# Kernel tuning notes

Measured on AMD Instinct MI355X. Metric: run time of the kernel, lower is better.

The kernel has to match this reference:

```python
import jax, jax.numpy as jnp
import numpy as np

# static config
B, H, W, C = 32, 56, 56, 128
WH, WW = 7, 7
SH, SW = 3, 3
NH = 4            # num heads
HD = C // NH      # head dim = 32
N = WH * WW       # 49 tokens per window
NWIN = (H // WH) * (W // WW)  # 64 windows
MLP_H = int(C * 4.0)
EPS = 1e-6
SCALE = HD ** -0.5


def _rel_pos_index():
    ch, cw = np.arange(WH), np.arange(WW)
    co = np.stack(np.meshgrid(ch, cw, indexing='ij')).reshape(2, -1)
    rc = (co[:, :, None] - co[:, None, :]).transpose(1, 2, 0)
    rc[:, :, 0] += WH - 1
    rc[:, :, 1] += WW - 1
    rc[:, :, 0] *= 2 * WW - 1
    return rc.sum(-1)  # [N, N] int


def _attn_mask():
    img = np.zeros((1, H, W, 1), np.float32)
    cnt = 0
    for hs in (slice(0, -WH), slice(-WH, -SH), slice(-SH, None)):
        for ws in (slice(0, -WW), slice(-WW, -SW), slice(-SW, None)):
            img[:, hs, ws, :] = cnt
            cnt += 1
    mw = img.reshape(1, H // WH, WH, W // WW, WW, 1)
    mw = mw.transpose(0, 1, 3, 2, 4, 5).reshape(-1, N)  # [nW, N]
    am = mw[:, None, :] - mw[:, :, None]
    return np.where(am != 0, -100.0, 0.0).astype(np.float32)  # [nW, N, N]

REL_IDX = jnp.asarray(_rel_pos_index())
ATTN_MASK = jnp.asarray(_attn_mask())


def _ln(x, g, b):
    mu = jnp.mean(x, -1, keepdims=True)
    var = jnp.mean(jnp.square(x - mu), -1, keepdims=True)
    return (x - mu) * jax.lax.rsqrt(var + EPS) * g + b


def _part(x):  # [B,H,W,C] -> [B*nW, N, C]
    x = x.reshape(B, H // WH, WH, W // WW, WW, C)
    return x.transpose(0, 1, 3, 2, 4, 5).reshape(-1, N, C)


def _rev(w):  # [B*nW, N, C] -> [B,H,W,C]
    x = w.reshape(B, H // WH, W // WW, WH, WW, C)
    return x.transpose(0, 1, 3, 2, 4, 5).reshape(B, H, W, C)


def setup_inputs() -> dict:
    key = jax.random.key(0)
    ks = jax.random.split(key, 16)
    s = lambda k, sh, sc=0.02: jax.random.normal(k, sh, jnp.float32) * sc
    return {
        'x': jax.random.normal(ks[0], (B, H * W, C), jnp.float32),
        'qkv_w': s(ks[1], (C, 3 * C)),
        'qkv_b': jnp.zeros((3 * C,), jnp.float32),
        'proj_w': s(ks[2], (C, C)),
        'proj_b': jnp.zeros((C,), jnp.float32),
        'proj_ln_g': jnp.ones((C,), jnp.float32),
        'proj_ln_b': jnp.zeros((C,), jnp.float32),
        'rpb_table': s(ks[3], ((2 * WH - 1) * (2 * WW - 1), NH)),
        'norm1_g': jnp.ones((C,), jnp.float32),
        'norm1_b': jnp.zeros((C,), jnp.float32),
        'norm2_g': jnp.ones((C,), jnp.float32),
        'norm2_b': jnp.zeros((C,), jnp.float32),
        'mlp_w1': s(ks[4], (C, MLP_H)),
        'mlp_b1': jnp.zeros((MLP_H,), jnp.float32),
        'mlp_w2': s(ks[5], (MLP_H, C)),
        'mlp_b2': jnp.zeros((C,), jnp.float32),
    }


def reference(x, qkv_w, qkv_b, proj_w, proj_b, proj_ln_g, proj_ln_b, rpb_table,
              norm1_g, norm1_b, norm2_g, norm2_b, mlp_w1, mlp_b1, mlp_w2, mlp_b2):
    shortcut = x
    h = _ln(x, norm1_g, norm1_b).reshape(B, H, W, C)
    h = jnp.roll(h, shift=(-SH, -SW), axis=(1, 2))        # cyclic shift
    w = _part(h)                                          # [B*nW, N, C]

    qkv = w @ qkv_w + qkv_b                               # [B*nW, N, 3C]
    qkv = qkv.reshape(-1, N, 3, NH, HD).transpose(2, 0, 3, 1, 4)
    q, k, v = qkv[0] * SCALE, qkv[1], qkv[2]              # [B*nW, NH, N, HD]
    attn = jnp.einsum('bhnd,bhmd->bhnm', q, k)            # [B*nW, NH, N, N]

    bias = rpb_table[REL_IDX.reshape(-1)].reshape(N, N, NH).transpose(2, 0, 1)
    attn = attn + bias[None]

    # masked path (shifted windows): NOTE source applies softmax TWICE — faithful
    attn = attn.reshape(-1, NWIN, NH, N, N) + ATTN_MASK[None, :, None]
    attn = jax.nn.softmax(attn, axis=-1)
    attn = attn.reshape(-1, NH, N, N)
    attn = jax.nn.softmax(attn, axis=-1)

    o = jnp.einsum('bhnm,bhmd->bhnd', attn, v)
    o = o.transpose(0, 2, 1, 3).reshape(-1, N, C)
    # projection: Dense -> LayerNorm -> GELU (as in source WindowAttention)
    o = jax.nn.gelu(_ln(o @ proj_w + proj_b, proj_ln_g, proj_ln_b), approximate=False)

    h = _rev(o)
    h = jnp.roll(h, shift=(SH, SW), axis=(1, 2)).reshape(B, H * W, C)
    x = shortcut + h

    m = _ln(x, norm2_g, norm2_b)
    m = jax.nn.gelu(m @ mlp_w1 + mlp_b1, approximate=False) @ mlp_w2 + mlp_b2
    return x + m
```

## Files before the change

kernel.cpp:

```cpp
#include <hip/hip_runtime.h>
#include <cstdint>
#include <cstddef>

typedef __attribute__((ext_vector_type(8))) short bf16x8;
typedef __attribute__((ext_vector_type(4))) float f32x4;

namespace {
constexpr float kScale = 0.17677669529663689f;
constexpr float kEps = 1e-6f;
constexpr float kInvC = 1.0f / 128.0f;

__device__ __forceinline__ float gelu_fast(float v) {
  float t1 = fmaf(0.044715f * v, v, 1.0f);
  float x = v * t1 * -1.5957691216057308f;
  float e = __expf(x);
  return v * __builtin_amdgcn_rcpf(1.0f + e);
}
__device__ __forceinline__ ushort f2bf(float f) {
  uint32_t u = __builtin_bit_cast(uint32_t, f);
  u += 0x7FFFu + ((u >> 16) & 1u);
  return (ushort)(u >> 16);
}
__device__ __forceinline__ float bf2f(ushort u) {
  return __builtin_bit_cast(float, (uint32_t)u << 16);
}
__device__ __forceinline__ void gl16(const ushort* g, ushort* l) {
  __builtin_amdgcn_global_load_lds(
      (const __attribute__((address_space(1))) void*)g,
      (__attribute__((address_space(3))) void*)l, 16, 0, 0);
}
__device__ __forceinline__ int map_row(int t) {
  int win = t / 49, nn = t - win * 49;
  int bb = win >> 6, wi = win & 63;
  int whi = wi >> 3, wwi = wi & 7;
  int r7 = nn / 7, c7 = nn - r7 * 7;
  int hs = whi * 7 + r7 + 3; if (hs >= 56) hs -= 56;
  int wsd = wwi * 7 + c7 + 3; if (wsd >= 56) wsd -= 56;
  return bb * 3136 + hs * 56 + wsd;
}
}

__global__ __launch_bounds__(256) void k_prep(
    const float* __restrict__ qkv_w, const float* __restrict__ w1,
    const float* __restrict__ w2, const float* __restrict__ pw,
    ushort* __restrict__ qkvT, ushort* __restrict__ w1T,
    ushort* __restrict__ w2T, ushort* __restrict__ projT) {
  int i = blockIdx.x * 256 + threadIdx.x;
  if (i < 49152) {
    int n = i >> 7, k = i & 127;
    qkvT[i] = f2bf(qkv_w[k * 384 + n]);
  } else if (i < 114688) {
    int j = i - 49152;
    int n = j >> 7, k = j & 127;
    w1T[j] = f2bf(w1[k * 512 + n]);
  } else if (i < 180224) {
    int j = i - 114688;
    int n = j >> 9, k = j & 511;
    w2T[j] = f2bf(w2[k * 128 + n]);
  } else if (i < 196608) {
    int j = i - 180224;
    int n = j >> 7, k = j & 127;
    projT[j] = f2bf(pw[k * 128 + n]);
  }
}

__global__ __launch_bounds__(256) void k_prep2(
    const float* __restrict__ rpb, float* __restrict__ TB) {
  int e = blockIdx.x * 256 + threadIdx.x;
  int i = e & 63, j = (e >> 6) & 63, h = (e >> 12) & 3, type = e >> 14;
  float v = 0.f;
  if (i < 49 && j < 49) {
    int ri = i / 7, ci = i - ri * 7, rj = j / 7, cj = j - rj * 7;
    int ridx = (ri - rj + 6) * 13 + (ci - cj + 6);
    float bias = rpb[ridx * 4 + h];
    int th = type >> 1, tw = type & 1;
    int labi = (th ? ((ri < 4) ? 1 : 2) : 0) * 3 + (tw ? ((ci < 4) ? 1 : 2) : 0);
    int labj = (th ? ((rj < 4) ? 1 : 2) : 0) * 3 + (tw ? ((cj < 4) ? 1 : 2) : 0);
    v = bias + ((labi != labj) ? -100.f : 0.f);
  }
  TB[e] = v;
}

__global__ __launch_bounds__(256) void k_ln1_part(
    const float* __restrict__ x, const float* __restrict__ g,
    const float* __restrict__ b, ushort* __restrict__ wp) {
  int lane = threadIdx.x & 63, wv = threadIdx.x >> 6;
  int half = lane >> 5, l32 = lane & 31;
  int tok = blockIdx.x * 8 + wv * 2 + half;
  size_t src = (size_t)map_row(tok) * 128;
  float4 v = *(const float4*)(x + src + l32 * 4);
  float s = v.x + v.y + v.z + v.w;
  float sq = v.x * v.x + v.y * v.y + v.z * v.z + v.w * v.w;
#pragma unroll
  for (int off = 1; off < 32; off <<= 1) {
    s += __shfl_xor(s, off);
    sq += __shfl_xor(sq, off);
  }
  float mu = s * kInvC;
  float var = sq * kInvC - mu * mu;
  float rs = rsqrtf(var + kEps);
  float4 gg = *(const float4*)(g + l32 * 4);
  float4 bv = *(const float4*)(b + l32 * 4);
  float o0 = (v.x - mu) * rs * gg.x + bv.x;
  float o1 = (v.y - mu) * rs * gg.y + bv.y;
  float o2 = (v.z - mu) * rs * gg.z + bv.z;
  float o3 = (v.w - mu) * rs * gg.w + bv.w;
  uint2 p;
  p.x = (uint)f2bf(o0) | ((uint)f2bf(o1) << 16);
  p.y = (uint)f2bf(o2) | ((uint)f2bf(o3) << 16);
  ((uint2*)wp)[(size_t)tok * 32 + l32] = p;
}

template <int K, int LDC, int EPI>
__global__ __launch_bounds__(256) void k_gemm2(
    const ushort* __restrict__ A, const ushort* __restrict__ BT,
    const float* __restrict__ bias, ushort* __restrict__ C) {
  __shared__ ushort sbuf[12288];
  int tid = threadIdx.x;
  int nBase = blockIdx.x << 7;
  int mBase = blockIdx.y << 6;
  int lane = tid & 63, wid = tid >> 6;
  int li = lane & 15, g = lane >> 4;
  int wr = (wid >> 1) << 5, wc = (wid & 1) << 6;
  int swz = (li & 7) << 3;
  f32x4 acc[2][4] = {};
  for (int ks = 0; ks < K; ks += 64) {
#pragma unroll
    for (int l = 0; l < 2; ++l) {
      int c = l * 256 + tid;
      int row = c >> 3;
      int k8 = ((c & 7) ^ (row & 7)) << 3;
      gl16(A + (size_t)(mBase + row) * K + ks + k8,
           sbuf + (l * 256 + wid * 64) * 8);
    }
#pragma unroll
    for (int l = 0; l < 4; ++l) {
      int c = l * 256 + tid;
      int row = c >> 3;
      int k8 = ((c & 7) ^ (row & 7)) << 3;
      gl16(BT + (size_t)(nBase + row) * K + ks + k8,
           sbuf + 4096 + (l * 256 + wid * 64) * 8);
    }
    __syncthreads();
#pragma unroll
    for (int ksub = 0; ksub < 64; ksub += 32) {
      int kloc = ksub + g * 8;
      bf16x8 af[2], bfr[4];
#pragma unroll
      for (int m = 0; m < 2; ++m)
        af[m] = *(const bf16x8*)(sbuf + (wr + m * 16 + li) * 64 + (kloc ^ swz));
#pragma unroll
      for (int n = 0; n < 4; ++n)
        bfr[n] = *(const bf16x8*)(sbuf + 4096 + (wc + n * 16 + li) * 64 +
                                  (kloc ^ swz));
#pragma unroll
      for (int m = 0; m < 2; ++m)
#pragma unroll
        for (int n = 0; n < 4; ++n)
          acc[m][n] = __builtin_amdgcn_mfma_f32_16x16x32_bf16(
              af[m], bfr[n], acc[m][n], 0, 0, 0);
    }
    __syncthreads();
  }
  ushort (*Cs)[128] = (ushort(*)[128])sbuf;
#pragma unroll
  for (int n = 0; n < 4; ++n) {
    float bv = bias[nBase + wc + n * 16 + li];
#pragma unroll
    for (int m = 0; m < 2; ++m) {
      int rb = wr + m * 16 + (g << 2);
#pragma unroll
      for (int r = 0; r < 4; ++r) {
        float v = acc[m][n][r] + bv;
        if (EPI == 1) v = gelu_fast(v);
        Cs[rb + r][wc + n * 16 + li] = f2bf(v);
      }
    }
  }
  __syncthreads();
#pragma unroll
  for (int it = 0; it < 4; ++it) {
    int ch = tid + it * 256;
    int row = ch >> 4, c8 = (ch & 15) << 3;
    *(bf16x8*)(C + (size_t)(mBase + row) * LDC + nBase + c8) =
        *(const bf16x8*)&Cs[row][c8];
  }
}

__global__ __launch_bounds__(256) void k_mlp2(
    const ushort* __restrict__ A, const ushort* __restrict__ BT,
    const float* __restrict__ bias, const ushort* __restrict__ resw,
    float* __restrict__ out) {
  __shared__ ushort sbuf[16384];
  __shared__ int mapr[64];
  int tid = threadIdx.x;
  int mBase = blockIdx.x << 6;
  if (tid < 64) mapr[tid] = map_row(mBase + tid);
  int lane = tid & 63, wid = tid >> 6;
  int li = lane & 15, g = lane >> 4;
  int wr = (wid >> 1) << 5, wc = (wid & 1) << 6;
  int swz = (li & 7) << 3;
  f32x4 acc[2][4] = {};
  for (int ks = 0; ks < 512; ks += 64) {
#pragma unroll
    for (int l = 0; l < 2; ++l) {
      int c = l * 256 + tid;
      int row = c >> 3;
      int k8 = ((c & 7) ^ (row & 7)) << 3;
      gl16(A + (size_t)(mBase + row) * 512 + ks + k8,
           sbuf + (l * 256 + wid * 64) * 8);
    }
#pragma unroll
    for (int l = 0; l < 4; ++l) {
      int c = l * 256 + tid;
      int row = c >> 3;
      int k8 = ((c & 7) ^ (row & 7)) << 3;
      gl16(BT + (size_t)row * 512 + ks + k8,
           sbuf + 4096 + (l * 256 + wid * 64) * 8);
    }
    __syncthreads();
#pragma unroll
    for (int ksub = 0; ksub < 64; ksub += 32) {
      int kloc = ksub + g * 8;
      bf16x8 af[2], bfr[4];
#pragma unroll
      for (int m = 0; m < 2; ++m)
        af[m] = *(const bf16x8*)(sbuf + (wr + m * 16 + li) * 64 + (kloc ^ swz));
#pragma unroll
      for (int n = 0; n < 4; ++n)
        bfr[n] = *(const bf16x8*)(sbuf + 4096 + (wc + n * 16 + li) * 64 +
                                  (kloc ^ swz));
#pragma unroll
      for (int m = 0; m < 2; ++m)
#pragma unroll
        for (int n = 0; n < 4; ++n)
          acc[m][n] = __builtin_amdgcn_mfma_f32_16x16x32_bf16(
              af[m], bfr[n], acc[m][n], 0, 0, 0);
    }
    __syncthreads();
  }
  float (*outs)[128] = (float(*)[128])sbuf;
#pragma unroll
  for (int n = 0; n < 4; ++n) {
    int cg = wc + n * 16 + li;
    float bv = bias[cg];
#pragma unroll
    for (int m = 0; m < 2; ++m) {
      int rb = wr + m * 16 + (g << 2);
#pragma unroll
      for (int r = 0; r < 4; ++r) {
        float rv = bf2f(resw[(size_t)(mBase + rb + r) * 128 + cg]);
        outs[rb + r][cg] = rv + acc[m][n][r] + bv;
      }
    }
  }
  __syncthreads();
#pragma unroll
  for (int it = 0; it < 8; ++it) {
    int ch = tid + it * 256;
    int row = ch >> 5, c4 = (ch & 31) << 2;
    *(float4*)(out + (size_t)mapr[row] * 128 + c4) =
        *(const float4*)&outs[row][c4];
  }
}

__global__ __launch_bounds__(256) void k_pgemm(
    const ushort* __restrict__ A, const ushort* __restrict__ BT,
    const float* __restrict__ pb, const float* __restrict__ lg,
    const float* __restrict__ lb, const float* __restrict__ x,
    const float* __restrict__ g2, const float* __restrict__ b2n,
    ushort* __restrict__ resw, ushort* __restrict__ wp) {
  __shared__ ushort sbuf[16384];
  __shared__ float red[4][64][2];
  __shared__ int mapr[64];
  int tid = threadIdx.x;
  int mBase = blockIdx.x << 6;
  if (tid < 64) mapr[tid] = map_row(mBase + tid);
  int lane = tid & 63, wid = tid >> 6;
  int li = lane & 15, g = lane >> 4;
  int wr = (wid >> 1) << 5, wc = (wid & 1) << 6;
  int swz = (li & 7) << 3;
  f32x4 acc[2][4] = {};
  for (int ks = 0; ks < 128; ks += 64) {
#pragma unroll
    for (int l = 0; l < 2; ++l) {
      int c = l * 256 + tid;
      int row = c >> 3;
      int k8 = ((c & 7) ^ (row & 7)) << 3;
      gl16(A + (size_t)(mBase + row) * 128 + ks + k8,
           sbuf + (l * 256 + wid * 64) * 8);
    }
#pragma unroll
    for (int l = 0; l < 4; ++l) {
      int c = l * 256 + tid;
      int row = c >> 3;
      int k8 = ((c & 7) ^ (row & 7)) << 3;
      gl16(BT + (size_t)row * 128 + ks + k8,
           sbuf + 4096 + (l * 256 + wid * 64) * 8);
    }
    __syncthreads();
#pragma unroll
    for (int ksub = 0; ksub < 64; ksub += 32) {
      int kloc = ksub + g * 8;
      bf16x8 af[2], bfr[4];
#pragma unroll
      for (int m = 0; m < 2; ++m)
        af[m] = *(const bf16x8*)(sbuf + (wr + m * 16 + li) * 64 + (kloc ^ swz));
#pragma unroll
      for (int n = 0; n < 4; ++n)
        bfr[n] = *(const bf16x8*)(sbuf + 4096 + (wc + n * 16 + li) * 64 +
                                  (kloc ^ swz));
#pragma unroll
      for (int m = 0; m < 2; ++m)
#pragma unroll
        for (int n = 0; n < 4; ++n)
          acc[m][n] = __builtin_amdgcn_mfma_f32_16x16x32_bf16(
              af[m], bfr[n], acc[m][n], 0, 0, 0);
    }
    __syncthreads();
  }
  float pbv[4], lgv[4], lbv[4], g2v[4], b2v[4];
#pragma unroll
  for (int n = 0; n < 4; ++n) {
    int cg = wc + n * 16 + li;
    pbv[n] = pb[cg]; lgv[n] = lg[cg]; lbv[n] = lb[cg];
    g2v[n] = g2[cg]; b2v[n] = b2n[cg];
  }
  float ps[2][4], psq[2][4];
#pragma unroll
  for (int m = 0; m < 2; ++m)
#pragma unroll
    for (int r = 0; r < 4; ++r) {
      float s = 0.f, q = 0.f;
#pragma unroll
      for (int n = 0; n < 4; ++n) {
        float v = acc[m][n][r] + pbv[n];
        s += v; q += v * v;
      }
#pragma unroll
      for (int off = 1; off < 16; off <<= 1) {
        s += __shfl_xor(s, off);
        q += __shfl_xor(q, off);
      }
      ps[m][r] = s; psq[m][r] = q;
    }
  if (li == 0) {
#pragma unroll
    for (int m = 0; m < 2; ++m)
#pragma unroll
      for (int r = 0; r < 4; ++r) {
        int rl = wr + m * 16 + (g << 2) + r;
        red[wid][rl][0] = ps[m][r];
        red[wid][rl][1] = psq[m][r];
      }
  }
  __syncthreads();
  float mu1[2][4], rs1[2][4];
#pragma unroll
  for (int m = 0; m < 2; ++m)
#pragma unroll
    for (int r = 0; r < 4; ++r) {
      int rl = wr + m * 16 + (g << 2) + r;
      float s = ps[m][r] + red[wid ^ 1][rl][0];
      float q = psq[m][r] + red[wid ^ 1][rl][1];
      mu1[m][r] = s * kInvC;
      rs1[m][r] = rsqrtf(q * kInvC - mu1[m][r] * mu1[m][r] + kEps);
    }
  __syncthreads();
#pragma unroll
  for (int m = 0; m < 2; ++m)
#pragma unroll
    for (int r = 0; r < 4; ++r) {
      int rowl = wr + m * 16 + (g << 2) + r;
      size_t xb = (size_t)mapr[rowl] * 128 + wc + li;
#pragma unroll
      for (int n = 0; n < 4; ++n) {
        float y = (acc[m][n][r] + pbv[n] - mu1[m][r]) * rs1[m][r] * lgv[n] +
                  lbv[n];
        acc[m][n][r] = gelu_fast(y) + x[xb + n * 16];
      }
    }
#pragma unroll
  for (int m = 0; m < 2; ++m)
#pragma unroll
    for (int r = 0; r < 4; ++r) {
      float s = 0.f, q = 0.f;
#pragma unroll
      for (int n = 0; n < 4; ++n) {
        float v = acc[m][n][r];
        s += v; q += v * v;
      }
#pragma unroll
      for (int off = 1; off < 16; off <<= 1) {
        s += __shfl_xor(s, off);
        q += __shfl_xor(q, off);
      }
      ps[m][r] = s; psq[m][r] = q;
    }
  if (li == 0) {
#pragma unroll
    for (int m = 0; m < 2; ++m)
#pragma unroll
      for (int r = 0; r < 4; ++r) {
        int rl = wr + m * 16 + (g << 2) + r;
        red[wid][rl][0] = ps[m][r];
        red[wid][rl][1] = psq[m][r];
      }
  }
  __syncthreads();
  ushort (*Cr)[128] = (ushort(*)[128])sbuf;
  ushort (*Cw)[128] = (ushort(*)[128])(sbuf + 8192);
#pragma unroll
  for (int m = 0; m < 2; ++m)
#pragma unroll
    for (int r = 0; r < 4; ++r) {
      int rl = wr + m * 16 + (g << 2) + r;
      float s = ps[m][r] + red[wid ^ 1][rl][0];
      float q = psq[m][r] + red[wid ^ 1][rl][1];
      float mu = s * kInvC;
      float rs = rsqrtf(q * kInvC - mu * mu + kEps);
#pragma unroll
      for (int n = 0; n < 4; ++n) {
        int col = wc + n * 16 + li;
        float rv = acc[m][n][r];
        Cr[rl][col] = f2bf(rv);
        Cw[rl][col] = f2bf((rv - mu) * rs * g2v[n] + b2v[n]);
      }
    }
  __syncthreads();
#pragma unroll
  for (int it = 0; it < 4; ++it) {
    int ch = tid + it * 256;
    int row = ch >> 4, c8 = (ch & 15) << 3;
    *(bf16x8*)(resw + (size_t)(mBase + row) * 128 + c8) =
        *(const bf16x8*)&Cr[row][c8];
    *(bf16x8*)(wp + (size_t)(mBase + row) * 128 + c8) =
        *(const bf16x8*)&Cw[row][c8];
  }
}

__global__ __launch_bounds__(256) void k_attn(
    const ushort* __restrict__ qkv, const float* __restrict__ TB,
    ushort* __restrict__ ob) {
  __shared__ ushort Pl[4][64][72];
  __shared__ ushort Vt[4][32][72];
  int tid = threadIdx.x;
  int lane = tid & 63, h = tid >> 6;
  int li = lane & 15, g = lane >> 4;
  int win = blockIdx.x;
  int wi = win & 63;
  int type = (((wi >> 3) == 7) ? 2 : 0) | (((wi & 7) == 7) ? 1 : 0);

  const ushort* qbase = qkv + (size_t)win * 49 * 384 + h * 32 + g * 8;
  bf16x8 kf[4], qf[4];
#pragma unroll
  for (int m = 0; m < 4; ++m) {
    kf[m] = *(const bf16x8*)(qbase + (size_t)(m * 16 + li) * 384 + 128);
    qf[m] = *(const bf16x8*)(qbase + (size_t)(m * 16 + li) * 384);
  }
  f32x4 zero = {0.f, 0.f, 0.f, 0.f};
  f32x4 st[4][4];
#pragma unroll
  for (int m = 0; m < 4; ++m)
#pragma unroll
    for (int n = 0; n < 4; ++n)
      st[m][n] = __builtin_amdgcn_mfma_f32_16x16x32_bf16(kf[m], qf[n], zero, 0, 0, 0);

  if (lane < 49) {
#pragma unroll
    for (int dc = 0; dc < 4; ++dc) {
      bf16x8 vv = *(const bf16x8*)(qkv + ((size_t)win * 49 + lane) * 384 + 256 +
                                   h * 32 + dc * 8);
#pragma unroll
      for (int t = 0; t < 8; ++t) Vt[h][dc * 8 + t][lane] = (ushort)vv[t];
    }
  } else {
#pragma unroll
    for (int d = 0; d < 32; ++d) Vt[h][d][lane] = 0;
  }

  const float* tb = TB + ((size_t)(type * 4 + h) << 12);
#pragma unroll
  for (int n = 0; n < 4; ++n) {
    int icol = n * 16 + li;
    float sv[3][4];
#pragma unroll
    for (int m = 0; m < 3; ++m)
#pragma unroll
      for (int r = 0; r < 4; ++r)
        sv[m][r] = st[m][n][r] * kScale + tb[(m * 16 + g * 4 + r) * 64 + icol];
    float sv3 = (g == 0) ? (st[3][n][0] * kScale + tb[48 * 64 + icol]) : -1e30f;
    float mx = sv3;
#pragma unroll
    for (int m = 0; m < 3; ++m)
#pragma unroll
      for (int r = 0; r < 4; ++r) mx = fmaxf(mx, sv[m][r]);
    mx = fmaxf(mx, __shfl_xor(mx, 16));
    mx = fmaxf(mx, __shfl_xor(mx, 32));
    float e[3][4], e3 = __expf(sv3 - mx);
    float sum = e3;
#pragma unroll
    for (int m = 0; m < 3; ++m)
#pragma unroll
      for (int r = 0; r < 4; ++r) { e[m][r] = __expf(sv[m][r] - mx); sum += e[m][r]; }
    sum += __shfl_xor(sum, 16);
    sum += __shfl_xor(sum, 32);
    float inv = 1.f / sum;
    float p3 = e3 * inv;
    float v3 = (g == 0) ? p3 : -1e30f;
    float mx2 = v3;
#pragma unroll
    for (int m = 0; m < 3; ++m)
#pragma unroll
      for (int r = 0; r < 4; ++r) mx2 = fmaxf(mx2, e[m][r] * inv);
    mx2 = fmaxf(mx2, __shfl_xor(mx2, 16));
    mx2 = fmaxf(mx2, __shfl_xor(mx2, 32));
    float e2[3][4], e23 = __expf(v3 - mx2);
    float sum2 = e23;
#pragma unroll
    for (int m = 0; m < 3; ++m)
#pragma unroll
      for (int r = 0; r < 4; ++r) { e2[m][r] = __expf(e[m][r] * inv - mx2); sum2 += e2[m][r]; }
    sum2 += __shfl_xor(sum2, 16);
    sum2 += __shfl_xor(sum2, 32);
    float inv2 = 1.f / sum2;
#pragma unroll
    for (int m = 0; m < 3; ++m) {
      uint u0 = (uint)f2bf(e2[m][0] * inv2) | ((uint)f2bf(e2[m][1] * inv2) << 16);
      uint u1 = (uint)f2bf(e2[m][2] * inv2) | ((uint)f2bf(e2[m][3] * inv2) << 16);
      *(uint*)&Pl[h][icol][m * 16 + g * 4]     = u0;
      *(uint*)&Pl[h][icol][m * 16 + g * 4 + 2] = u1;
    }
    uint u3 = (uint)f2bf(e23 * inv2);
    *(uint*)&Pl[h][icol][48 + g * 4]     = u3;
    *(uint*)&Pl[h][icol][48 + g * 4 + 2] = 0u;
  }
  __syncthreads();

  f32x4 oacc[4][2] = {};
#pragma unroll
  for (int ks = 0; ks < 2; ++ks) {
    int kloc = ks * 32 + g * 8;
    bf16x8 bf0 = *(const bf16x8*)&Vt[h][li][kloc];
    bf16x8 bf1 = *(const bf16x8*)&Vt[h][16 + li][kloc];
#pragma unroll
    for (int mi = 0; mi < 4; ++mi) {
      bf16x8 af = *(const bf16x8*)&Pl[h][mi * 16 + li][kloc];
      oacc[mi][0] = __builtin_amdgcn_mfma_f32_16x16x32_bf16(af, bf0, oacc[mi][0], 0, 0, 0);
      oacc[mi][1] = __builtin_amdgcn_mfma_f32_16x16x32_bf16(af, bf1, oacc[mi][1], 0, 0, 0);
    }
  }
  ushort* OlH = &Pl[h][0][0];
#pragma unroll
  for (int mi = 0; mi < 4; ++mi)
#pragma unroll
    for (int r = 0; r < 4; ++r) {
      int i = mi * 16 + g * 4 + r;
      if (mi < 3 || (g == 0 && r == 0)) {
        OlH[i * 40 + li]      = f2bf(oacc[mi][0][r]);
        OlH[i * 40 + 16 + li] = f2bf(oacc[mi][1][r]);
      }
    }
  __syncthreads();
  ushort* obase = ob + (size_t)win * 49 * 128;
#pragma unroll
  for (int it = 0; it < 4; ++it) {
    int chunk = tid + it * 256;
    if (chunk < 784) {
      int row = chunk >> 4, c8 = (chunk & 15) << 3;
      int h2 = c8 >> 5, d8 = c8 & 31;
      bf16x8 v = *(const bf16x8*)(&Pl[h2][0][0] + row * 40 + d8);
      *(bf16x8*)(obase + (size_t)row * 128 + c8) = v;
    }
  }
}

extern "C" void kernel_launch(void* const* d_in, const int* in_sizes, int n_in,
                              void* d_out, int out_size, void* d_ws,
                              size_t ws_size, hipStream_t stream) {
  (void)in_sizes; (void)n_in; (void)out_size; (void)ws_size;
  const float* x      = (const float*)d_in[0];
  const float* qkv_w  = (const float*)d_in[1];
  const float* qkv_b  = (const float*)d_in[2];
  const float* proj_w = (const float*)d_in[3];
  const float* proj_b = (const float*)d_in[4];
  const float* plg    = (const float*)d_in[5];
  const float* plb    = (const float*)d_in[6];
  const float* rpb    = (const float*)d_in[7];
  const float* n1g    = (const float*)d_in[8];
  const float* n1b    = (const float*)d_in[9];
  const float* n2g    = (const float*)d_in[10];
  const float* n2b    = (const float*)d_in[11];
  const float* w1     = (const float*)d_in[12];
  const float* b1     = (const float*)d_in[13];
  const float* w2     = (const float*)d_in[14];
  const float* b2     = (const float*)d_in[15];
  float* out = (float*)d_out;

  ushort* wp   = (ushort*)d_ws;
  ushort* qkvb = wp + (size_t)100352 * 128;
  ushort* obb  = qkvb + (size_t)100352 * 384;
  ushort* hb   = obb + (size_t)100352 * 128;
  ushort* qkvT = hb + (size_t)100352 * 512;
  ushort* w1T  = qkvT + 384 * 128;
  ushort* w2T  = w1T + 512 * 128;
  ushort* pT   = w2T + 128 * 512;
  float*  TB   = (float*)(pT + 128 * 128);
  ushort* resw = qkvb;

  k_prep<<<768, 256, 0, stream>>>(qkv_w, w1, w2, proj_w, qkvT, w1T, w2T, pT);
  k_prep2<<<256, 256, 0, stream>>>(rpb, TB);
  k_ln1_part<<<12544, 256, 0, stream>>>(x, n1g, n1b, wp);
  k_gemm2<128, 384, 0><<<dim3(3, 1568), 256, 0, stream>>>(wp, qkvT, qkv_b, qkvb);
  k_attn<<<2048, 256, 0, stream>>>(qkvb, TB, obb);
  k_pgemm<<<1568, 256, 0, stream>>>(obb, pT, proj_b, plg, plb, x, n2g, n2b,
                                    resw, wp);
  k_gemm2<128, 512, 1><<<dim3(4, 1568), 256, 0, stream>>>(wp, w1T, b1, hb);
  k_mlp2<<<1568, 256, 0, stream>>>(hb, w2T, b2, resw, out);
}
```

Baseline: 200.7 us.

## Store MLP hidden activations and W2 in FP8 and use FP8 MFMA for MLP2

The first MLP GEMM now writes its GELU output as FP8 (e4m3) instead of bf16, and W2 is pre-converted to FP8. The second MLP GEMM loads these byte-wide operands and runs fp8 x fp8 MFMA, halving the hidden-activation traffic and LDS footprint per K step. It trades numerical precision in the MLP for lower memory bandwidth on the largest intermediate tensor, which may exceed the accuracy tolerance.

```diff
diff --git a/kernel.cpp b/kernel.cpp
--- a/kernel.cpp
+++ b/kernel.cpp
@@ -4,6 +4,7 @@
 
 typedef __attribute__((ext_vector_type(8))) short bf16x8;
 typedef __attribute__((ext_vector_type(4))) float f32x4;
+typedef unsigned char uchar;
 
 namespace {
 constexpr float kScale = 0.17677669529663689f;
@@ -24,7 +25,7 @@
 __device__ __forceinline__ float bf2f(ushort u) {
   return __builtin_bit_cast(float, (uint32_t)u << 16);
 }
-__device__ __forceinline__ void gl16(const ushort* g, ushort* l) {
+__device__ __forceinline__ void gl16(const void* g, void* l) {
   __builtin_amdgcn_global_load_lds(
       (const __attribute__((address_space(1))) void*)g,
       (__attribute__((address_space(3))) void*)l, 16, 0, 0);
@@ -44,7 +45,7 @@
     const float* __restrict__ qkv_w, const float* __restrict__ w1,
     const float* __restrict__ w2, const float* __restrict__ pw,
     ushort* __restrict__ qkvT, ushort* __restrict__ w1T,
-    ushort* __restrict__ w2T, ushort* __restrict__ projT) {
+    uchar* __restrict__ w2T8, ushort* __restrict__ projT) {
   int i = blockIdx.x * 256 + threadIdx.x;
   if (i < 49152) {
     int n = i >> 7, k = i & 127;
@@ -53,12 +54,16 @@
     int j = i - 49152;
     int n = j >> 7, k = j & 127;
     w1T[j] = f2bf(w1[k * 512 + n]);
-  } else if (i < 180224) {
+  } else if (i < 147456) {
     int j = i - 114688;
-    int n = j >> 9, k = j & 511;
-    w2T[j] = f2bf(w2[k * 128 + n]);
-  } else if (i < 196608) {
-    int j = i - 180224;
+    int n = j >> 8, k2 = (j & 255) << 1;
+    int u = __builtin_amdgcn_cvt_pk_fp8_f32(w2[(size_t)k2 * 128 + n],
+                                            w2[(size_t)(k2 + 1) * 128 + n], 0,
+                                            false);
+    w2T8[n * 512 + k2] = (uchar)u;
+    w2T8[n * 512 + k2 + 1] = (uchar)(u >> 8);
+  } else if (i < 163840) {
+    int j = i - 147456;
     int n = j >> 7, k = j & 127;
     projT[j] = f2bf(pw[k * 128 + n]);
   }
@@ -187,11 +192,91 @@
   }
 }
 
+__global__ __launch_bounds__(256) void k_mlp1(
+    const ushort* __restrict__ A, const ushort* __restrict__ BT,
+    const float* __restrict__ bias, uchar* __restrict__ C8) {
+  __shared__ ushort sbuf[12288];
+  int tid = threadIdx.x;
+  int nBase = blockIdx.x << 7;
+  int mBase = blockIdx.y << 6;
+  int lane = tid & 63, wid = tid >> 6;
+  int li = lane & 15, g = lane >> 4;
+  int wr = (wid >> 1) << 5, wc = (wid & 1) << 6;
+  int swz = (li & 7) << 3;
+  f32x4 acc[2][4] = {};
+  for (int ks = 0; ks < 128; ks += 64) {
+#pragma unroll
+    for (int l = 0; l < 2; ++l) {
+      int c = l * 256 + tid;
+      int row = c >> 3;
+      int k8 = ((c & 7) ^ (row & 7)) << 3;
+      gl16(A + (size_t)(mBase + row) * 128 + ks + k8,
+           sbuf + (l * 256 + wid * 64) * 8);
+    }
+#pragma unroll
+    for (int l = 0; l < 4; ++l) {
+      int c = l * 256 + tid;
+      int row = c >> 3;
+      int k8 = ((c & 7) ^ (row & 7)) << 3;
+      gl16(BT + (size_t)(nBase + row) * 128 + ks + k8,
+           sbuf + 4096 + (l * 256 + wid * 64) * 8);
+    }
+    __syncthreads();
+#pragma unroll
+    for (int ksub = 0; ksub < 64; ksub += 32) {
+      int kloc = ksub + g * 8;
+      bf16x8 af[2], bfr[4];
+#pragma unroll
+      for (int m = 0; m < 2; ++m)
+        af[m] = *(const bf16x8*)(sbuf + (wr + m * 16 + li) * 64 + (kloc ^ swz));
+#pragma unroll
+      for (int n = 0; n < 4; ++n)
+        bfr[n] = *(const bf16x8*)(sbuf + 4096 + (wc + n * 16 + li) * 64 +
+                                  (kloc ^ swz));
+#pragma unroll
+      for (int m = 0; m < 2; ++m)
+#pragma unroll
+        for (int n = 0; n < 4; ++n)
+          acc[m][n] = __builtin_amdgcn_mfma_f32_16x16x32_bf16(
+              af[m], bfr[n], acc[m][n], 0, 0, 0);
+    }
+    __syncthreads();
+  }
+  uchar (*Cs8)[128] = (uchar(*)[128])sbuf;
+#pragma unroll
+  for (int n = 0; n < 4; ++n) {
+    float bv = bias[nBase + wc + n * 16 + li];
+    int col = wc + n * 16 + li;
+#pragma unroll
+    for (int m = 0; m < 2; ++m) {
+      int rb = wr + m * 16 + (g << 2);
+      float v0 = gelu_fast(acc[m][n][0] + bv);
+      float v1 = gelu_fast(acc[m][n][1] + bv);
+      float v2 = gelu_fast(acc[m][n][2] + bv);
+      float v3 = gelu_fast(acc[m][n][3] + bv);
+      int u01 = __builtin_amdgcn_cvt_pk_fp8_f32(v0, v1, 0, false);
+      int u23 = __builtin_amdgcn_cvt_pk_fp8_f32(v2, v3, 0, false);
+      Cs8[rb + 0][col] = (uchar)u01;
+      Cs8[rb + 1][col] = (uchar)(u01 >> 8);
+      Cs8[rb + 2][col] = (uchar)u23;
+      Cs8[rb + 3][col] = (uchar)(u23 >> 8);
+    }
+  }
+  __syncthreads();
+#pragma unroll
+  for (int it = 0; it < 2; ++it) {
+    int ch = tid + it * 256;
+    int row = ch >> 3, c16 = (ch & 7) << 4;
+    *(bf16x8*)(C8 + (size_t)(mBase + row) * 512 + nBase + c16) =
+        *(const bf16x8*)&Cs8[row][c16];
+  }
+}
+
 __global__ __launch_bounds__(256) void k_mlp2(
-    const ushort* __restrict__ A, const ushort* __restrict__ BT,
+    const uchar* __restrict__ A8, const uchar* __restrict__ BT8,
     const float* __restrict__ bias, const ushort* __restrict__ resw,
     float* __restrict__ out) {
-  __shared__ ushort sbuf[16384];
+  __shared__ uchar sbuf[32768];
   __shared__ int mapr[64];
   int tid = threadIdx.x;
   int mBase = blockIdx.x << 6;
@@ -199,42 +284,45 @@
   int lane = tid & 63, wid = tid >> 6;
   int li = lane & 15, g = lane >> 4;
   int wr = (wid >> 1) << 5, wc = (wid & 1) << 6;
-  int swz = (li & 7) << 3;
   f32x4 acc[2][4] = {};
-  for (int ks = 0; ks < 512; ks += 64) {
+  for (int kb = 0; kb < 512; kb += 128) {
 #pragma unroll
     for (int l = 0; l < 2; ++l) {
       int c = l * 256 + tid;
       int row = c >> 3;
-      int k8 = ((c & 7) ^ (row & 7)) << 3;
-      gl16(A + (size_t)(mBase + row) * 512 + ks + k8,
-           sbuf + (l * 256 + wid * 64) * 8);
+      int ch = (c & 7) ^ (row & 7);
+      gl16(A8 + (size_t)(mBase + row) * 512 + kb + (ch << 4),
+           sbuf + (l * 256 + wid * 64) * 16);
     }
 #pragma unroll
     for (int l = 0; l < 4; ++l) {
       int c = l * 256 + tid;
       int row = c >> 3;
-      int k8 = ((c & 7) ^ (row & 7)) << 3;
-      gl16(BT + (size_t)row * 512 + ks + k8,
-           sbuf + 4096 + (l * 256 + wid * 64) * 8);
+      int ch = (c & 7) ^ (row & 7);
+      gl16(BT8 + (size_t)row * 512 + kb + (ch << 4),
+           sbuf + 8192 + (l * 256 + wid * 64) * 16);
     }
     __syncthreads();
 #pragma unroll
-    for (int ksub = 0; ksub < 64; ksub += 32) {
-      int kloc = ksub + g * 8;
-      bf16x8 af[2], bfr[4];
+    for (int ks = 0; ks < 4; ++ks) {
+      int off = ks * 32 + g * 8;
+      long long af[2], bfr[4];
+#pragma unroll
+      for (int m = 0; m < 2; ++m) {
+        int r = wr + m * 16 + li;
+        af[m] = *(const long long*)(sbuf + r * 128 + (off ^ ((r & 7) << 4)));
+      }
+#pragma unroll
+      for (int n = 0; n < 4; ++n) {
+        int rb = wc + n * 16 + li;
+        bfr[n] = *(const long long*)(sbuf + 8192 + rb * 128 +
+                                     (off ^ ((rb & 7) << 4)));
+      }
 #pragma unroll
       for (int m = 0; m < 2; ++m)
-        af[m] = *(const bf16x8*)(sbuf + (wr + m * 16 + li) * 64 + (kloc ^ swz));
-#pragma unroll
-      for (int n = 0; n < 4; ++n)
-        bfr[n] = *(const bf16x8*)(sbuf + 4096 + (wc + n * 16 + li) * 64 +
-                                  (kloc ^ swz));
-#pragma unroll
-      for (int m = 0; m < 2; ++m)
 #pragma unroll
         for (int n = 0; n < 4; ++n)
-          acc[m][n] = __builtin_amdgcn_mfma_f32_16x16x32_bf16(
+          acc[m][n] = __builtin_amdgcn_mfma_f32_16x16x32_fp8_fp8(
               af[m], bfr[n], acc[m][n], 0, 0, 0);
     }
     __syncthreads();
@@ -600,21 +688,21 @@
   ushort* wp   = (ushort*)d_ws;
   ushort* qkvb = wp + (size_t)100352 * 128;
   ushort* obb  = qkvb + (size_t)100352 * 384;
-  ushort* hb   = obb + (size_t)100352 * 128;
-  ushort* qkvT = hb + (size_t)100352 * 512;
+  uchar*  hb8  = (uchar*)(obb + (size_t)100352 * 128);
+  ushort* qkvT = (ushort*)(hb8 + (size_t)100352 * 512);
   ushort* w1T  = qkvT + 384 * 128;
-  ushort* w2T  = w1T + 512 * 128;
-  ushort* pT   = w2T + 128 * 512;
+  uchar*  w2T8 = (uchar*)(w1T + 512 * 128);
+  ushort* pT   = (ushort*)(w2T8 + 128 * 512);
   float*  TB   = (float*)(pT + 128 * 128);
   ushort* resw = qkvb;
 
-  k_prep<<<768, 256, 0, stream>>>(qkv_w, w1, w2, proj_w, qkvT, w1T, w2T, pT);
+  k_prep<<<640, 256, 0, stream>>>(qkv_w, w1, w2, proj_w, qkvT, w1T, w2T8, pT);
   k_prep2<<<256, 256, 0, stream>>>(rpb, TB);
   k_ln1_part<<<12544, 256, 0, stream>>>(x, n1g, n1b, wp);
   k_gemm2<128, 384, 0><<<dim3(3, 1568), 256, 0, stream>>>(wp, qkvT, qkv_b, qkvb);
   k_attn<<<2048, 256, 0, stream>>>(qkvb, TB, obb);
   k_pgemm<<<1568, 256, 0, stream>>>(obb, pT, proj_b, plg, plb, x, n2g, n2b,
                                     resw, wp);
-  k_gemm2<128, 512, 1><<<dim3(4, 1568), 256, 0, stream>>>(wp, w1T, b1, hb);
-  k_mlp2<<<1568, 256, 0, stream>>>(hb, w2T, b2, resw, out);
-}
+  k_mlp1<<<dim3(4, 1568), 256, 0, stream>>>(wp, w1T, b1, hb8);
+  k_mlp2<<<1568, 256, 0, stream>>>(hb8, w2T8, b2, resw, out);
+}
```

Result: faster. 177.9 us (-11.3%).
